# Kernel tuning notes

Measured on AMD Instinct MI355X. Metric: run time of the kernel, lower is better.

The kernel has to match this reference:

```python
import jax, jax.numpy as jnp
import numpy as np

# LinearQuantWLog hyperparameters (from init_kwargs)
GAMMA = 2.0
INIT = 0.25
SIZE = 5
N_TOKENS = 262144
IN_FEATURES = 256
OUT_FEATURES = 256


def exp_proj(w):
    """Project weights onto the logarithmic grid {sign(w) * INIT * GAMMA**k, k=0..SIZE-1}.

    Mirrors elastic_quant_connect.exp_proj used by QuantLogDense: round the
    base-GAMMA log of |w|/INIT, clamp the exponent to [0, SIZE-1].
    """
    log_g = jnp.log(jnp.abs(w) / INIT) / jnp.log(GAMMA)
    k = jnp.clip(jnp.round(log_g), 0.0, SIZE - 1.0)  # -inf at w==0 clips to 0; sign(0)=0 kills it
    return jnp.sign(w) * (INIT * jnp.power(GAMMA, k))


def setup_inputs() -> dict:
    key = jax.random.key(0)
    k_in, k_w = jax.random.split(key)
    wmax = INIT * GAMMA ** (SIZE - 1)  # reset_parameters uniform range
    inputs = {
        "input": jax.random.normal(k_in, (N_TOKENS, IN_FEATURES), dtype=jnp.float32),
        "weight": jax.random.uniform(k_w, (OUT_FEATURES, IN_FEATURES), dtype=jnp.float32,
                                     minval=-wmax, maxval=wmax),
        "bias": jnp.zeros((OUT_FEATURES,), dtype=jnp.float32),
    }
    return inputs


def reference(input, weight, bias):
    # Quantize weights to the log grid, then dense matmul (F.linear semantics).
    w_q = exp_proj(weight)  # [out, in]
    return jnp.dot(input, w_q.T) + bias  # [N, out]
```

## Files before the change

kernel.cpp:

```cpp
#include <hip/hip_runtime.h>
#include <hip/hip_bf16.h>
#include <stdint.h>

typedef float  f32x4  __attribute__((ext_vector_type(4)));
typedef __bf16 bf16x8 __attribute__((ext_vector_type(8)));
typedef __bf16 bf16x4 __attribute__((ext_vector_type(4)));
typedef unsigned int u32;
typedef u32 u32v2 __attribute__((ext_vector_type(2)));

#define GRID   1024
#define MROWS  32
#define ITERS  8
#define ROWB   528
#define TILEB  (MROWS * ROWB)
#define WSB    65536

#define BAR() do {                                         \
    asm volatile("s_waitcnt lgkmcnt(0)" ::: "memory");     \
    __builtin_amdgcn_s_barrier();                          \
} while (0)

__device__ __forceinline__ float qlog(float v) {
    float a = fabsf(v);
    int k = (a >= 0.35355339059327373f)
          + (a >= 0.70710678118654746f)
          + (a >= 1.41421356237309515f)
          + (a >= 2.82842712474619029f);
    float q = 0.25f * (float)(1 << k);
    return (v == 0.0f) ? 0.0f : copysignf(q, v);
}

__device__ __forceinline__ u32 enc1(float q) {
    u32 b16 = __float_as_uint(q) >> 16;
    return b16 ? (((b16 >> 8) & 0x80u) | (((b16 >> 7) & 0xFFu) - 64u)) : 0u;
}

__device__ __forceinline__ u32 dec2(u32 d) {
    u32 t = d & 0x00800080u;
    return (d + t + 0x00400040u) << 7;
}
__device__ __forceinline__ bf16x8 dec_frag(u32 c0, u32 c1) {
#if __has_builtin(__builtin_amdgcn_perm)
    u32 d0 = __builtin_amdgcn_perm(0u, c0, 0x0C010C00u);
    u32 d1 = __builtin_amdgcn_perm(0u, c0, 0x0C030C02u);
    u32 d2 = __builtin_amdgcn_perm(0u, c1, 0x0C010C00u);
    u32 d3 = __builtin_amdgcn_perm(0u, c1, 0x0C030C02u);
#else
    u32 d0 = (c0 & 0xFFu) | ((c0 & 0xFF00u) << 8);
    u32 d1 = ((c0 >> 16) & 0xFFu) | ((c0 & 0xFF000000u) >> 8);
    u32 d2 = (c1 & 0xFFu) | ((c1 & 0xFF00u) << 8);
    u32 d3 = ((c1 >> 16) & 0xFFu) | ((c1 & 0xFF000000u) >> 8);
#endif
    union { u32 u[4]; bf16x8 v; } u_;
    u_.u[0] = dec2(d0); u_.u[1] = dec2(d1);
    u_.u[2] = dec2(d2); u_.u[3] = dec2(d3);
    return u_.v;
}

__global__ __launch_bounds__(256) void lqw_quant(
    const float* __restrict__ w, u32v2* __restrict__ wsq)
{
    const int gid  = blockIdx.x * 256 + threadIdx.x;
    const int lane = gid & 63;
    const int kt   = (gid >> 6) & 7;
    const int ntv  = gid >> 9;
    const float* src = w + (size_t)(ntv * 16 + (lane & 15)) * 256
                         + kt * 32 + (lane >> 4) * 8;
    u32v2 c = (u32v2){0, 0};
    #pragma unroll
    for (int e = 0; e < 4; ++e) c[0] |= enc1(qlog(src[e]))     << (8 * e);
    #pragma unroll
    for (int e = 0; e < 4; ++e) c[1] |= enc1(qlog(src[4 + e])) << (8 * e);
    wsq[gid] = c;
    __threadfence();
}

template<bool USE_WS>
__global__ __launch_bounds__(512, 4) void lqw_gemm(
    const float* __restrict__ in,
    const float* __restrict__ w,
    const float* __restrict__ bias,
    const u32v2* __restrict__ wsq,
    float* __restrict__ out)
{
    __shared__ __align__(16) char smem[2 * TILEB];
    const int tid  = threadIdx.x;
    const int lane = tid & 63;
    const int wv   = tid >> 6;
    const int nbase = wv * 32;
    const int lrow = lane & 15;
    const int kgrp = lane >> 4;

    u32v2 bc[2][8];
    if (USE_WS) {
        #pragma unroll
        for (int nt = 0; nt < 2; ++nt)
            #pragma unroll
            for (int kt = 0; kt < 8; ++kt)
                bc[nt][kt] = wsq[(size_t)((wv * 2 + nt) * 8 + kt) * 64 + lane];
    } else {
        #pragma unroll
        for (int nt = 0; nt < 2; ++nt) {
            const float* wrow = w + (size_t)(nbase + nt * 16 + lrow) * 256;
            #pragma unroll
            for (int kt = 0; kt < 8; ++kt) {
                u32v2 c = (u32v2){0, 0};
                #pragma unroll
                for (int e = 0; e < 4; ++e)
                    c[0] |= enc1(qlog(wrow[kt * 32 + kgrp * 8 + e])) << (8 * e);
                #pragma unroll
                for (int e = 0; e < 4; ++e)
                    c[1] |= enc1(qlog(wrow[kt * 32 + kgrp * 8 + 4 + e])) << (8 * e);
                bc[nt][kt] = c;
            }
        }
    }
    f32x4 bv[2];
    #pragma unroll
    for (int nt = 0; nt < 2; ++nt)
        bv[nt] = *(const f32x4*)(bias + nbase + nt * 16 + kgrp * 4);

    const int mt0 = blockIdx.x * ITERS;

    #define LOAD_TILE(S, mt) do {                                          \
        const f32x4* _s = (const f32x4*)(in + (size_t)(mt) * (MROWS*256)); \
        S[0] = _s[0*512 + tid]; S[1] = _s[1*512 + tid];                    \
        S[2] = _s[2*512 + tid]; S[3] = _s[3*512 + tid];                    \
    } while (0)

    #define WRITE_TILE(b, S) do {                                          \
        char* _d = smem + (b) * TILEB;                                     \
        _Pragma("unroll")                                                  \
        for (int r = 0; r < 4; ++r) {                                      \
            int j = r * 512 + tid;                                         \
            bf16x4 v;                                                      \
            v[0] = (__bf16)S[r][0]; v[1] = (__bf16)S[r][1];                \
            v[2] = (__bf16)S[r][2]; v[3] = (__bf16)S[r][3];                \
            *(bf16x4*)(_d + (j >> 6) * ROWB + (j & 63) * 8) = v;           \
        }                                                                  \
    } while (0)

    #define COMPUTE(b, mt) do {                                                             \
        const char* base = smem + (b) * TILEB;                                              \
        f32x4 acc[2][2];                                                                    \
        _Pragma("unroll")                                                                   \
        for (int mi = 0; mi < 2; ++mi)                                                      \
            _Pragma("unroll")                                                               \
            for (int nt = 0; nt < 2; ++nt) acc[mi][nt] = bv[nt];                            \
        _Pragma("unroll")                                                                   \
        for (int kt = 0; kt < 8; ++kt) {                                                    \
            bf16x8 a0 = *(const bf16x8*)(base + (size_t)lrow * ROWB + kt * 64 + kgrp * 16); \
            bf16x8 a1 = *(const bf16x8*)(base + (size_t)(16 + lrow) * ROWB + kt * 64 + kgrp * 16); \
            bf16x8 b0 = dec_frag(bc[0][kt][0], bc[0][kt][1]);                               \
            bf16x8 b1 = dec_frag(bc[1][kt][0], bc[1][kt][1]);                               \
            acc[0][0] = __builtin_amdgcn_mfma_f32_16x16x32_bf16(b0, a0, acc[0][0], 0, 0, 0); \
            acc[0][1] = __builtin_amdgcn_mfma_f32_16x16x32_bf16(b1, a0, acc[0][1], 0, 0, 0); \
            acc[1][0] = __builtin_amdgcn_mfma_f32_16x16x32_bf16(b0, a1, acc[1][0], 0, 0, 0); \
            acc[1][1] = __builtin_amdgcn_mfma_f32_16x16x32_bf16(b1, a1, acc[1][1], 0, 0, 0); \
        }                                                                                   \
        _Pragma("unroll")                                                                   \
        for (int mi = 0; mi < 2; ++mi) {                                                    \
            float* orow = out + (size_t)((mt) * 32 + mi * 16 + lrow) * 256 + nbase + kgrp * 4; \
            *(f32x4*)(orow)      = acc[mi][0];                                              \
            *(f32x4*)(orow + 16) = acc[mi][1];                                              \
        }                                                                                   \
    } while (0)

    f32x4 sA[4], sB[4];
    LOAD_TILE(sA, mt0);
    LOAD_TILE(sB, mt0 + 1);
    WRITE_TILE(0, sA);
    LOAD_TILE(sA, mt0 + 2);
    BAR();

    #pragma unroll 1
    for (int t = 0; t < ITERS; t += 2) {
        WRITE_TILE(1, sB);
        if (t + 3 < ITERS) LOAD_TILE(sB, mt0 + t + 3);
        COMPUTE(0, mt0 + t);
        BAR();
        if (t + 2 < ITERS) WRITE_TILE(0, sA);
        if (t + 4 < ITERS) LOAD_TILE(sA, mt0 + t + 4);
        COMPUTE(1, mt0 + t + 1);
        BAR();
    }
}

extern "C" void kernel_launch(void* const* d_in, const int* in_sizes, int n_in,
                              void* d_out, int out_size, void* d_ws, size_t ws_size,
                              hipStream_t stream) {
    const float* in_p   = (const float*)d_in[0];
    const float* w_p    = (const float*)d_in[1];
    const float* bias_p = (const float*)d_in[2];
    float* out_p        = (float*)d_out;
    if (ws_size >= WSB) {
        u32v2* wsq = (u32v2*)d_ws;
        lqw_quant<<<32, 256, 0, stream>>>(w_p, wsq);
        lqw_gemm<true><<<GRID, 512, 0, stream>>>(in_p, w_p, bias_p, wsq, out_p);
    } else {
        lqw_gemm<false><<<GRID, 512, 0, stream>>>(in_p, w_p, bias_p, nullptr, out_p);
    }
}
```

Before: 136.8 us.

## Stream fp32 input tiles directly into swizzled LDS via global_load_lds

The activation tile is no longer staged through registers with a bf16 conversion. It is copied straight from global memory into LDS as fp32 using global_load_lds, with an XOR swizzle on the 16-byte chunks. Conversion to bf16 now happens when the MFMA fragments are read from LDS. The pipeline becomes a simple double buffer with one barrier per tile. The aim is to cut VGPR use and the issue cost of staging, at the price of twice the LDS per tile, which may lower occupancy, and more conversion work inside the compute loop.

```diff
diff --git a/kernel.cpp b/kernel.cpp
--- a/kernel.cpp
+++ b/kernel.cpp
@@ -4,21 +4,14 @@
 
 typedef float  f32x4  __attribute__((ext_vector_type(4)));
 typedef __bf16 bf16x8 __attribute__((ext_vector_type(8)));
-typedef __bf16 bf16x4 __attribute__((ext_vector_type(4)));
 typedef unsigned int u32;
 typedef u32 u32v2 __attribute__((ext_vector_type(2)));
 
 #define GRID   1024
 #define MROWS  32
 #define ITERS  8
-#define ROWB   528
-#define TILEB  (MROWS * ROWB)
+#define TILEB  (MROWS * 1024)
 #define WSB    65536
-
-#define BAR() do {                                         \
-    asm volatile("s_waitcnt lgkmcnt(0)" ::: "memory");     \
-    __builtin_amdgcn_s_barrier();                          \
-} while (0)
 
 __device__ __forceinline__ float qlog(float v) {
     float a = fabsf(v);
@@ -34,7 +27,6 @@
     u32 b16 = __float_as_uint(q) >> 16;
     return b16 ? (((b16 >> 8) & 0x80u) | (((b16 >> 7) & 0xFFu) - 64u)) : 0u;
 }
-
 __device__ __forceinline__ u32 dec2(u32 d) {
     u32 t = d & 0x00800080u;
     return (d + t + 0x00400040u) << 7;
@@ -57,6 +49,17 @@
     return u_.v;
 }
 
+__device__ __forceinline__ void gload16(const float* g, char* l) {
+#if __has_builtin(__builtin_amdgcn_global_load_lds)
+    __builtin_amdgcn_global_load_lds(
+        (const __attribute__((address_space(1))) u32*)g,
+        (__attribute__((address_space(3))) u32*)l, 16, 0, 0);
+#else
+    const int lane = threadIdx.x & 63;
+    *(f32x4*)(l + lane * 16) = *(const f32x4*)(g + lane * 4);
+#endif
+}
+
 __global__ __launch_bounds__(256) void lqw_quant(
     const float* __restrict__ w, u32v2* __restrict__ wsq)
 {
@@ -90,6 +93,9 @@
     const int nbase = wv * 32;
     const int lrow = lane & 15;
     const int kgrp = lane >> 4;
+    const int s    = lrow & 7;
+    const int o0 = ((kgrp * 2)     ^ s) * 16;
+    const int o1 = ((kgrp * 2 + 1) ^ s) * 16;
 
     u32v2 bc[2][8];
     if (USE_WS) {
@@ -122,22 +128,15 @@
 
     const int mt0 = blockIdx.x * ITERS;
 
-    #define LOAD_TILE(S, mt) do {                                          \
-        const f32x4* _s = (const f32x4*)(in + (size_t)(mt) * (MROWS*256)); \
-        S[0] = _s[0*512 + tid]; S[1] = _s[1*512 + tid];                    \
-        S[2] = _s[2*512 + tid]; S[3] = _s[3*512 + tid];                    \
-    } while (0)
-
-    #define WRITE_TILE(b, S) do {                                          \
-        char* _d = smem + (b) * TILEB;                                     \
-        _Pragma("unroll")                                                  \
-        for (int r = 0; r < 4; ++r) {                                      \
-            int j = r * 512 + tid;                                         \
-            bf16x4 v;                                                      \
-            v[0] = (__bf16)S[r][0]; v[1] = (__bf16)S[r][1];                \
-            v[2] = (__bf16)S[r][2]; v[3] = (__bf16)S[r][3];                \
-            *(bf16x4*)(_d + (j >> 6) * ROWB + (j & 63) * 8) = v;           \
-        }                                                                  \
+    #define STAGE(b, mt) do {                                               \
+        char* _d = smem + (b) * TILEB;                                      \
+        _Pragma("unroll")                                                   \
+        for (int j = 0; j < 4; ++j) {                                       \
+            const int r = wv * 4 + j;                                       \
+            const float* _s = in + ((size_t)(mt) * MROWS + r) * 256         \
+                                 + ((lane ^ (r & 7)) << 2);                 \
+            gload16(_s, _d + r * 1024);                                     \
+        }                                                                   \
     } while (0)
 
     #define COMPUTE(b, mt) do {                                                             \
@@ -147,10 +146,20 @@
         for (int mi = 0; mi < 2; ++mi)                                                      \
             _Pragma("unroll")                                                               \
             for (int nt = 0; nt < 2; ++nt) acc[mi][nt] = bv[nt];                            \
+        const char* row0 = base + (size_t)lrow * 1024;                                      \
+        const char* row1 = base + (size_t)(16 + lrow) * 1024;                               \
         _Pragma("unroll")                                                                   \
         for (int kt = 0; kt < 8; ++kt) {                                                    \
-            bf16x8 a0 = *(const bf16x8*)(base + (size_t)lrow * ROWB + kt * 64 + kgrp * 16); \
-            bf16x8 a1 = *(const bf16x8*)(base + (size_t)(16 + lrow) * ROWB + kt * 64 + kgrp * 16); \
+            f32x4 lo0 = *(const f32x4*)(row0 + kt * 128 + o0);                              \
+            f32x4 hi0 = *(const f32x4*)(row0 + kt * 128 + o1);                              \
+            f32x4 lo1 = *(const f32x4*)(row1 + kt * 128 + o0);                              \
+            f32x4 hi1 = *(const f32x4*)(row1 + kt * 128 + o1);                              \
+            bf16x8 a0, a1;                                                                  \
+            _Pragma("unroll")                                                               \
+            for (int e = 0; e < 4; ++e) {                                                   \
+                a0[e] = (__bf16)lo0[e]; a0[4 + e] = (__bf16)hi0[e];                         \
+                a1[e] = (__bf16)lo1[e]; a1[4 + e] = (__bf16)hi1[e];                         \
+            }                                                                               \
             bf16x8 b0 = dec_frag(bc[0][kt][0], bc[0][kt][1]);                               \
             bf16x8 b1 = dec_frag(bc[1][kt][0], bc[1][kt][1]);                               \
             acc[0][0] = __builtin_amdgcn_mfma_f32_16x16x32_bf16(b0, a0, acc[0][0], 0, 0, 0); \
@@ -160,29 +169,25 @@
         }                                                                                   \
         _Pragma("unroll")                                                                   \
         for (int mi = 0; mi < 2; ++mi) {                                                    \
-            float* orow = out + (size_t)((mt) * 32 + mi * 16 + lrow) * 256 + nbase + kgrp * 4; \
+            float* orow = out + (size_t)((mt) * MROWS + mi * 16 + lrow) * 256 + nbase + kgrp * 4; \
             *(f32x4*)(orow)      = acc[mi][0];                                              \
             *(f32x4*)(orow + 16) = acc[mi][1];                                              \
         }                                                                                   \
     } while (0)
 
-    f32x4 sA[4], sB[4];
-    LOAD_TILE(sA, mt0);
-    LOAD_TILE(sB, mt0 + 1);
-    WRITE_TILE(0, sA);
-    LOAD_TILE(sA, mt0 + 2);
-    BAR();
+    STAGE(0, mt0);
+    asm volatile("s_waitcnt vmcnt(0)" ::: "memory");
+    __builtin_amdgcn_s_barrier();
 
     #pragma unroll 1
-    for (int t = 0; t < ITERS; t += 2) {
-        WRITE_TILE(1, sB);
-        if (t + 3 < ITERS) LOAD_TILE(sB, mt0 + t + 3);
-        COMPUTE(0, mt0 + t);
-        BAR();
-        if (t + 2 < ITERS) WRITE_TILE(0, sA);
-        if (t + 4 < ITERS) LOAD_TILE(sA, mt0 + t + 4);
-        COMPUTE(1, mt0 + t + 1);
-        BAR();
+    for (int t = 0; t < ITERS; ++t) {
+        const int b = t & 1;
+        if (t + 1 < ITERS) STAGE(b ^ 1, mt0 + t + 1);
+        __builtin_amdgcn_sched_barrier(0);
+        COMPUTE(b, mt0 + t);
+        asm volatile("s_waitcnt vmcnt(4) lgkmcnt(0)" ::: "memory");
+        __builtin_amdgcn_sched_barrier(0);
+        __builtin_amdgcn_s_barrier();
     }
 }
 
```

Result: faster. 115.6 us (-15.5%).
